# Kernel tuning notes

Hardware: AMD Instinct MI355X
Metric: run time of the kernel (lower is better)

Reference implementation:

```python
import jax, jax.numpy as jnp
import numpy as np

N_NODES = 50000
N_EDGES = 800000


def gcn_conv(x, W, b, src, dst, n):
    """PyG-style GCNConv: add self-loops, symmetric deg normalization,
    out[i] = sum_{j->i} deg[i]^-1/2 deg[j]^-1/2 (x @ W)[j] + b."""
    h = x @ W                                   # [n, d_out]
    loop = jnp.arange(n, dtype=src.dtype)
    s = jnp.concatenate([src, loop])            # sources incl self-loops
    d = jnp.concatenate([dst, loop])            # destinations incl self-loops
    deg = jax.ops.segment_sum(jnp.ones_like(d, dtype=h.dtype), d, num_segments=n)
    dinv = jax.lax.rsqrt(jnp.maximum(deg, 1.0))
    norm = dinv[s] * dinv[d]                    # [E+n]
    msg = norm[:, None] * h[s]                  # gather + scale, [E+n, d_out]
    out = jax.ops.segment_sum(msg, d, num_segments=n)  # scatter-add
    return out + b


def setup_inputs() -> dict:
    key = jax.random.key(0)
    ks = jax.random.split(key, 8)
    x = jax.random.normal(ks[0], (N_NODES, 128), dtype=jnp.float32)
    edge_index = jax.random.randint(ks[1], (2, N_EDGES), 0, N_NODES, dtype=jnp.int64)
    def glorot(k, shape):
        lim = np.sqrt(6.0 / (shape[0] + shape[1])).astype(np.float32)
        return jax.random.uniform(k, shape, dtype=jnp.float32, minval=-lim, maxval=lim)
    return {
        "x": x,
        "edge_index": edge_index,
        "W1": glorot(ks[2], (128, 128)), "b1": jnp.zeros((128,), jnp.float32),
        "W2": glorot(ks[3], (128, 64)),  "b2": jnp.zeros((64,), jnp.float32),
        "W3": glorot(ks[4], (64, 16)),   "b3": jnp.zeros((16,), jnp.float32),
    }


def reference(x, edge_index, W1, b1, W2, b2, W3, b3):
    src, dst = edge_index[0], edge_index[1]
    n = x.shape[0]
    # base_model: 2-layer GCN
    h = gcn_conv(x, W1, b1, src, dst, n)
    h = jax.nn.relu(h)
    h = gcn_conv(h, W2, b2, src, dst, n)
    # added layer + softmax over class dim
    logits = gcn_conv(h, W3, b3, src, dst, n)
    return jax.nn.softmax(logits, axis=1)
```

## Files before the change

### kernel.cpp

```cpp
#include <hip/hip_runtime.h>
#include <hip/hip_fp16.h>

#define CAP 64


__global__ __launch_bounds__(256) void k_scatter_p(const int* __restrict__ src,
                                                   const int* __restrict__ dst,
                                                   int* __restrict__ cnt,
                                                   unsigned short* __restrict__ srcS,
                                                   int E) {
    int e = blockIdx.x * 256 + threadIdx.x;
    if (e >= E) return;
    int d = dst[e];
    int pos = atomicAdd(&cnt[d], 1);
    if (pos < CAP) srcS[(size_t)d * CAP + pos] = (unsigned short)src[e];
}

__global__ __launch_bounds__(256) void k_dinv(const int* __restrict__ cnt,
                                              float* __restrict__ dinv, int n) {
    int i = blockIdx.x * 256 + threadIdx.x;
    if (i < n) dinv[i] = rsqrtf((float)cnt[i] + 1.0f);
}


template<int DIN, int DOUT, int TM, int TN, int KC>
__global__ __launch_bounds__(256) void k_gemm2h(const float* __restrict__ X,
                                                const float* __restrict__ W,
                                                const float* __restrict__ dinv,
                                                __half* __restrict__ Y, int n) {
    constexpr int CG = DOUT / TN;
    constexpr int RG = 256 / CG;
    constexpr int TILE_R = RG * TM;
    constexpr int NCHUNK = DIN / KC;
    constexpr int XS = KC + 4;
    __shared__ float wsh[KC * DOUT];
    __shared__ float xs[TILE_R * XS];

    const int rb = blockIdx.x * TILE_R;
    const int cg = threadIdx.x % CG;
    const int rg = threadIdx.x / CG;
    const int c0 = cg * TN;
    const int r0 = rg * TM;

    float acc[TM][TN] = {};

    for (int kc = 0; kc < NCHUNK; ++kc) {
        const int k0 = kc * KC;
        const float4* wg = reinterpret_cast<const float4*>(W + (size_t)k0 * DOUT);
        for (int i = threadIdx.x; i < KC * DOUT / 4; i += 256)
            reinterpret_cast<float4*>(wsh)[i] = wg[i];
        for (int i = threadIdx.x; i < TILE_R * KC / 4; i += 256) {
            int r = i / (KC / 4);
            int kk = (i % (KC / 4)) * 4;
            int row = rb + r;
            float4 v = {0.f, 0.f, 0.f, 0.f};
            if (row < n) v = *reinterpret_cast<const float4*>(X + (size_t)row * DIN + k0 + kk);
            *reinterpret_cast<float4*>(&xs[r * XS + kk]) = v;
        }
        __syncthreads();
#pragma unroll 4
        for (int k = 0; k < KC; ++k) {
            float wr[TN], xr[TM];
#pragma unroll
            for (int j = 0; j < TN; j += 4)
                *reinterpret_cast<float4*>(&wr[j]) =
                    *reinterpret_cast<const float4*>(&wsh[k * DOUT + c0 + j]);
#pragma unroll
            for (int i = 0; i < TM; ++i) xr[i] = xs[(r0 + i) * XS + k];
#pragma unroll
            for (int i = 0; i < TM; ++i)
#pragma unroll
                for (int j = 0; j < TN; ++j)
                    acc[i][j] = fmaf(xr[i], wr[j], acc[i][j]);
        }
        __syncthreads();
    }

#pragma unroll
    for (int i = 0; i < TM; ++i) {
        int row = rb + r0 + i;
        if (row < n) {
            float di = dinv[row];
            union { float4 f4; float2 f2[2]; __half h[8]; } u;
#pragma unroll
            for (int j = 0; j < TN; ++j) u.h[j] = __float2half_rn(acc[i][j] * di);
            __half* yp = Y + (size_t)row * DOUT + c0;
            if (TN == 8) *reinterpret_cast<float4*>(yp) = u.f4;
            else         *reinterpret_cast<float2*>(yp) = u.f2[0];
        }
    }
}


template<int DQ, int MODE>
__global__ __launch_bounds__(256) void k_gather_h(const __half* __restrict__ tmp,
                                                  const int* __restrict__ cnt,
                                                  const unsigned short* __restrict__ srcS,
                                                  const float* __restrict__ dinv,
                                                  const float* __restrict__ b,
                                                  float* __restrict__ out, int n) {
    int tid = blockIdx.x * 256 + threadIdx.x;
    int i = tid / DQ;
    if (i >= n) return;
    int c = tid % DQ;
    const float4* t4 = reinterpret_cast<const float4*>(tmp);
    float acc[8];
    {
        float4 v = t4[(size_t)i * DQ + c];
        const __half2* h = reinterpret_cast<const __half2*>(&v);
#pragma unroll
        for (int q = 0; q < 4; ++q) {
            float2 f = __half22float2(h[q]);
            acc[2 * q] = f.x; acc[2 * q + 1] = f.y;
        }
    }
    const int e1 = cnt[i];
    const unsigned short* sp = srcS + (size_t)i * CAP;
#pragma unroll 4
    for (int e = 0; e < e1; ++e) {
        int s = sp[e];
        float4 v = t4[(size_t)s * DQ + c];
        const __half2* h = reinterpret_cast<const __half2*>(&v);
#pragma unroll
        for (int q = 0; q < 4; ++q) {
            float2 f = __half22float2(h[q]);
            acc[2 * q] += f.x; acc[2 * q + 1] += f.y;
        }
    }
    const float di = dinv[i];
    float r[8];
    const float* bp = b + c * 8;
#pragma unroll
    for (int q = 0; q < 8; ++q) r[q] = di * acc[q] + bp[q];
    if (MODE == 1) {
#pragma unroll
        for (int q = 0; q < 8; ++q) r[q] = fmaxf(r[q], 0.f);
    }
    if (MODE == 2) {
        float m = r[0];
#pragma unroll
        for (int q = 1; q < 8; ++q) m = fmaxf(m, r[q]);
        m = fmaxf(m, __shfl_xor(m, 1, 2));
        float s = 0.f;
#pragma unroll
        for (int q = 0; q < 8; ++q) { r[q] = __expf(r[q] - m); s += r[q]; }
        s += __shfl_xor(s, 1, 2);
        float inv = 1.f / s;
#pragma unroll
        for (int q = 0; q < 8; ++q) r[q] *= inv;
    }
    float4* o4 = reinterpret_cast<float4*>(out + ((size_t)i * DQ + c) * 8);
    float4 w0 = {r[0], r[1], r[2], r[3]};
    float4 w1 = {r[4], r[5], r[6], r[7]};
    o4[0] = w0; o4[1] = w1;
}


extern "C" void kernel_launch(void* const* d_in, const int* in_sizes, int n_in,
                              void* d_out, int out_size, void* d_ws, size_t ws_size,
                              hipStream_t stream) {
    const float* x  = (const float*)d_in[0];
    const int*   ei = (const int*)d_in[1];
    const float* W1 = (const float*)d_in[2];
    const float* b1 = (const float*)d_in[3];
    const float* W2 = (const float*)d_in[4];
    const float* b2 = (const float*)d_in[5];
    const float* W3 = (const float*)d_in[6];
    const float* b3 = (const float*)d_in[7];

    const int n = in_sizes[0] / 128;
    const int E = in_sizes[1] / 2;
    const int* srcp = ei;
    const int* dstp = ei + E;

    auto align = [](size_t v) { return (v + 255) & ~(size_t)255; };
    char* ws = (char*)d_ws;
    size_t o = 0;
    float*          dinv = (float*)(ws + o);          o += align((size_t)n * 4);
    int*            cnt  = (int*)(ws + o);            o += align((size_t)n * 4);
    unsigned short* srcS = (unsigned short*)(ws + o); o += align((size_t)n * CAP * 2);
    __half*         bufA = (__half*)(ws + o);         o += align((size_t)n * 128 * 2);
    float*          bufB = (float*)(ws + o);

    auto cdiv = [](long long a, long long b) { return (int)((a + b - 1) / b); };

    hipMemsetAsync(cnt, 0, (size_t)n * 4, stream);
    k_scatter_p<<<cdiv(E, 256), 256, 0, stream>>>(srcp, dstp, cnt, srcS, E);
    k_dinv<<<cdiv(n, 256), 256, 0, stream>>>(cnt, dinv, n);

    k_gemm2h<128, 128, 4, 8, 64><<<cdiv(n, 64), 256, 0, stream>>>(x, W1, dinv, bufA, n);
    k_gather_h<16, 1><<<cdiv((long long)n * 16, 256), 256, 0, stream>>>(
        bufA, cnt, srcS, dinv, b1, bufB, n);

    k_gemm2h<128, 64, 4, 4, 64><<<cdiv(n, 64), 256, 0, stream>>>(bufB, W2, dinv, bufA, n);
    k_gather_h<8, 0><<<cdiv((long long)n * 8, 256), 256, 0, stream>>>(
        bufA, cnt, srcS, dinv, b2, bufB, n);

    k_gemm2h<64, 16, 4, 4, 64><<<cdiv(n, 256), 256, 0, stream>>>(bufB, W3, dinv, bufA, n);
    k_gather_h<2, 2><<<cdiv((long long)n * 2, 256), 256, 0, stream>>>(
        bufA, cnt, srcS, dinv, b3, (float*)d_out, n);
}
```

Baseline: 254.3 us.

## Fuse edge scatter into first GEMM launch and defer dinv scaling

The edge bucketing scatter and the first-layer GEMM now run in one launch, with block ranges split by role, so the atomic-heavy scatter overlaps with the GEMM compute. The GEMM no longer depends on dinv. A new kernel computes dinv and rescales the fp16 GEMM output in place. The GEMM K-chunk also shrinks from 64 to 32, lowering shared memory use. The trade-off is an extra read-modify-write pass over the fp16 buffer and a second fp16 rounding of the intermediate values.

```diff
diff --git a/kernel.cpp b/kernel.cpp
--- a/kernel.cpp
+++ b/kernel.cpp
@@ -4,22 +4,107 @@
 #define CAP 64
 
 
-__global__ __launch_bounds__(256) void k_scatter_p(const int* __restrict__ src,
-                                                   const int* __restrict__ dst,
-                                                   int* __restrict__ cnt,
-                                                   unsigned short* __restrict__ srcS,
-                                                   int E) {
-    int e = blockIdx.x * 256 + threadIdx.x;
-    if (e >= E) return;
-    int d = dst[e];
-    int pos = atomicAdd(&cnt[d], 1);
-    if (pos < CAP) srcS[(size_t)d * CAP + pos] = (unsigned short)src[e];
-}
-
-__global__ __launch_bounds__(256) void k_dinv(const int* __restrict__ cnt,
-                                              float* __restrict__ dinv, int n) {
-    int i = blockIdx.x * 256 + threadIdx.x;
-    if (i < n) dinv[i] = rsqrtf((float)cnt[i] + 1.0f);
+template<int DIN, int DOUT, int TM, int TN, int KC, int EPB>
+__global__ __launch_bounds__(256) void k_fused1(const float* __restrict__ X,
+                                                const float* __restrict__ W,
+                                                __half* __restrict__ Y, int n, int G_gemm,
+                                                const int* __restrict__ src,
+                                                const int* __restrict__ dst,
+                                                int* __restrict__ cnt,
+                                                unsigned short* __restrict__ srcS, int E) {
+    constexpr int CG = DOUT / TN;
+    constexpr int RG = 256 / CG;
+    constexpr int TILE_R = RG * TM;
+    constexpr int NCHUNK = DIN / KC;
+    constexpr int XS = KC + 4;
+    __shared__ float wsh[KC * DOUT];
+    __shared__ float xs[TILE_R * XS];
+
+    if (blockIdx.x >= G_gemm) {
+        int base = (blockIdx.x - G_gemm) * 256 * EPB + threadIdx.x;
+#pragma unroll
+        for (int k = 0; k < EPB; ++k) {
+            int e = base + k * 256;
+            if (e < E) {
+                int d = dst[e];
+                int pos = atomicAdd(&cnt[d], 1);
+                if (pos < CAP) srcS[(size_t)d * CAP + pos] = (unsigned short)src[e];
+            }
+        }
+        return;
+    }
+
+    const int rb = blockIdx.x * TILE_R;
+    const int cg = threadIdx.x % CG;
+    const int rg = threadIdx.x / CG;
+    const int c0 = cg * TN;
+    const int r0 = rg * TM;
+
+    float acc[TM][TN] = {};
+
+    for (int kc = 0; kc < NCHUNK; ++kc) {
+        const int k0 = kc * KC;
+        const float4* wg = reinterpret_cast<const float4*>(W + (size_t)k0 * DOUT);
+        for (int i = threadIdx.x; i < KC * DOUT / 4; i += 256)
+            reinterpret_cast<float4*>(wsh)[i] = wg[i];
+        for (int i = threadIdx.x; i < TILE_R * KC / 4; i += 256) {
+            int r = i / (KC / 4);
+            int kk = (i % (KC / 4)) * 4;
+            int row = rb + r;
+            float4 v = {0.f, 0.f, 0.f, 0.f};
+            if (row < n) v = *reinterpret_cast<const float4*>(X + (size_t)row * DIN + k0 + kk);
+            *reinterpret_cast<float4*>(&xs[r * XS + kk]) = v;
+        }
+        __syncthreads();
+#pragma unroll 4
+        for (int k = 0; k < KC; ++k) {
+            float wr[TN], xr[TM];
+#pragma unroll
+            for (int j = 0; j < TN; j += 4)
+                *reinterpret_cast<float4*>(&wr[j]) =
+                    *reinterpret_cast<const float4*>(&wsh[k * DOUT + c0 + j]);
+#pragma unroll
+            for (int i = 0; i < TM; ++i) xr[i] = xs[(r0 + i) * XS + k];
+#pragma unroll
+            for (int i = 0; i < TM; ++i)
+#pragma unroll
+                for (int j = 0; j < TN; ++j)
+                    acc[i][j] = fmaf(xr[i], wr[j], acc[i][j]);
+        }
+        __syncthreads();
+    }
+
+#pragma unroll
+    for (int i = 0; i < TM; ++i) {
+        int row = rb + r0 + i;
+        if (row < n) {
+            union { float4 f4; __half h[8]; } u;
+#pragma unroll
+            for (int j = 0; j < TN; ++j) u.h[j] = __float2half_rn(acc[i][j]);
+            *reinterpret_cast<float4*>(Y + (size_t)row * DOUT + c0) = u.f4;
+        }
+    }
+}
+
+
+__global__ __launch_bounds__(256) void k_dinv_scale(const int* __restrict__ cnt,
+                                                    float* __restrict__ dinv,
+                                                    __half* __restrict__ t, int n) {
+    int tid = blockIdx.x * 256 + threadIdx.x;
+    int i = tid / 16;
+    if (i >= n) return;
+    int c = tid % 16;
+    float di = rsqrtf((float)cnt[i] + 1.0f);
+    if (c == 0) dinv[i] = di;
+    float4 v = reinterpret_cast<float4*>(t)[(size_t)i * 16 + c];
+    __half2* h = reinterpret_cast<__half2*>(&v);
+#pragma unroll
+    for (int q = 0; q < 4; ++q) {
+        float2 f = __half22float2(h[q]);
+        f.x *= di; f.y *= di;
+        h[q] = __float22half2_rn(f);
+    }
+    reinterpret_cast<float4*>(t)[(size_t)i * 16 + c] = v;
 }
 
 
@@ -185,10 +270,14 @@
     auto cdiv = [](long long a, long long b) { return (int)((a + b - 1) / b); };
 
     hipMemsetAsync(cnt, 0, (size_t)n * 4, stream);
-    k_scatter_p<<<cdiv(E, 256), 256, 0, stream>>>(srcp, dstp, cnt, srcS, E);
-    k_dinv<<<cdiv(n, 256), 256, 0, stream>>>(cnt, dinv, n);
-
-    k_gemm2h<128, 128, 4, 8, 64><<<cdiv(n, 64), 256, 0, stream>>>(x, W1, dinv, bufA, n);
+
+    const int G_gemm = cdiv(n, 64);
+    const int G_scat = cdiv(E, 256 * 2);
+    k_fused1<128, 128, 4, 8, 32, 2><<<G_gemm + G_scat, 256, 0, stream>>>(
+        x, W1, bufA, n, G_gemm, srcp, dstp, cnt, srcS, E);
+
+    k_dinv_scale<<<cdiv((long long)n * 16, 256), 256, 0, stream>>>(cnt, dinv, bufA, n);
+
     k_gather_h<16, 1><<<cdiv((long long)n * 16, 256), 256, 0, stream>>>(
         bufA, cnt, srcS, dinv, b1, bufB, n);
 
```

After: 222.6 us. 12.4% less time.

## Fuse edge scatter into first GEMM and gather-aggregation into next-layer GEMMs

Applied to the files above, without the earlier changes.

Runs the edge bucketing as extra blocks of the first GEMM launch and drops the separate dinv kernel. Degree normalization is now computed inline with rsqrt from the counts, and the source-side dinv is applied per edge during the layer-1 gather. Layers 1 and 2 aggregate into shared memory and immediately multiply by the next weight matrix, so fp32 intermediate activations never go to global memory. This cuts the launch count from eight kernels to four and removes those round trips. The cost is one extra cnt lookup per edge in the first gather, and a first GEMM with a smaller K chunk.

```diff
diff --git a/kernel.cpp b/kernel.cpp
--- a/kernel.cpp
+++ b/kernel.cpp
@@ -4,30 +4,14 @@
 #define CAP 64
 
 
-__global__ __launch_bounds__(256) void k_scatter_p(const int* __restrict__ src,
-                                                   const int* __restrict__ dst,
-                                                   int* __restrict__ cnt,
-                                                   unsigned short* __restrict__ srcS,
-                                                   int E) {
-    int e = blockIdx.x * 256 + threadIdx.x;
-    if (e >= E) return;
-    int d = dst[e];
-    int pos = atomicAdd(&cnt[d], 1);
-    if (pos < CAP) srcS[(size_t)d * CAP + pos] = (unsigned short)src[e];
-}
-
-__global__ __launch_bounds__(256) void k_dinv(const int* __restrict__ cnt,
-                                              float* __restrict__ dinv, int n) {
-    int i = blockIdx.x * 256 + threadIdx.x;
-    if (i < n) dinv[i] = rsqrtf((float)cnt[i] + 1.0f);
-}
-
-
-template<int DIN, int DOUT, int TM, int TN, int KC>
-__global__ __launch_bounds__(256) void k_gemm2h(const float* __restrict__ X,
+template<int DIN, int DOUT, int TM, int TN, int KC, int EPB>
+__global__ __launch_bounds__(256) void k_fused1(const float* __restrict__ X,
                                                 const float* __restrict__ W,
-                                                const float* __restrict__ dinv,
-                                                __half* __restrict__ Y, int n) {
+                                                __half* __restrict__ Y, int n, int G_gemm,
+                                                const int* __restrict__ src,
+                                                const int* __restrict__ dst,
+                                                int* __restrict__ cnt,
+                                                unsigned short* __restrict__ srcS, int E) {
     constexpr int CG = DOUT / TN;
     constexpr int RG = 256 / CG;
     constexpr int TILE_R = RG * TM;
@@ -35,6 +19,20 @@
     constexpr int XS = KC + 4;
     __shared__ float wsh[KC * DOUT];
     __shared__ float xs[TILE_R * XS];
+
+    if (blockIdx.x >= G_gemm) {
+        int base = (blockIdx.x - G_gemm) * 256 * EPB + threadIdx.x;
+#pragma unroll
+        for (int k = 0; k < EPB; ++k) {
+            int e = base + k * 256;
+            if (e < E) {
+                int d = dst[e];
+                int pos = atomicAdd(&cnt[d], 1);
+                if (pos < CAP) srcS[(size_t)d * CAP + pos] = (unsigned short)src[e];
+            }
+        }
+        return;
+    }
 
     const int rb = blockIdx.x * TILE_R;
     const int cg = threadIdx.x % CG;
@@ -80,78 +78,222 @@
     for (int i = 0; i < TM; ++i) {
         int row = rb + r0 + i;
         if (row < n) {
-            float di = dinv[row];
-            union { float4 f4; float2 f2[2]; __half h[8]; } u;
-#pragma unroll
-            for (int j = 0; j < TN; ++j) u.h[j] = __float2half_rn(acc[i][j] * di);
-            __half* yp = Y + (size_t)row * DOUT + c0;
-            if (TN == 8) *reinterpret_cast<float4*>(yp) = u.f4;
-            else         *reinterpret_cast<float2*>(yp) = u.f2[0];
-        }
-    }
-}
-
-
-template<int DQ, int MODE>
-__global__ __launch_bounds__(256) void k_gather_h(const __half* __restrict__ tmp,
+            union { float4 f4; __half h[8]; } u;
+#pragma unroll
+            for (int j = 0; j < TN; ++j) u.h[j] = __float2half_rn(acc[i][j]);
+            *reinterpret_cast<float4*>(Y + (size_t)row * DOUT + c0) = u.f4;
+        }
+    }
+}
+
+
+__global__ __launch_bounds__(256) void k_g1_gemm2(const __half* __restrict__ t1,
                                                   const int* __restrict__ cnt,
                                                   const unsigned short* __restrict__ srcS,
-                                                  const float* __restrict__ dinv,
-                                                  const float* __restrict__ b,
-                                                  float* __restrict__ out, int n) {
+                                                  const float* __restrict__ b1,
+                                                  const float* __restrict__ W2,
+                                                  __half* __restrict__ t2, int n) {
+    __shared__ float h_sh[32][132];
+    __shared__ float wsh[32 * 64];
+    const int rb = blockIdx.x * 32;
+    const int tid = threadIdx.x;
+    const int c = tid & 15;
+    const int gl = tid >> 4;
+
+    for (int pass = 0; pass < 2; ++pass) {
+        const int lrow = pass * 16 + gl;
+        const int i = rb + lrow;
+        if (i < n) {
+            const int ci = cnt[i];
+            const float di = rsqrtf((float)ci + 1.0f);
+            float acc[8];
+            float4 v = reinterpret_cast<const float4*>(t1)[(size_t)i * 16 + c];
+            const __half2* hp = reinterpret_cast<const __half2*>(&v);
+#pragma unroll
+            for (int q = 0; q < 4; ++q) {
+                float2 f = __half22float2(hp[q]);
+                acc[2 * q] = di * f.x; acc[2 * q + 1] = di * f.y;
+            }
+            const int e1 = min(ci, CAP);
+            const unsigned short* sp = srcS + (size_t)i * CAP;
+#pragma unroll 4
+            for (int e = 0; e < e1; ++e) {
+                int s = sp[e];
+                float ds = rsqrtf((float)cnt[s] + 1.0f);
+                float4 w = reinterpret_cast<const float4*>(t1)[(size_t)s * 16 + c];
+                const __half2* wp = reinterpret_cast<const __half2*>(&w);
+#pragma unroll
+                for (int q = 0; q < 4; ++q) {
+                    float2 f = __half22float2(wp[q]);
+                    acc[2 * q]     = fmaf(ds, f.x, acc[2 * q]);
+                    acc[2 * q + 1] = fmaf(ds, f.y, acc[2 * q + 1]);
+                }
+            }
+#pragma unroll
+            for (int q = 0; q < 8; ++q) {
+                float r = fmaf(di, acc[q], b1[c * 8 + q]);
+                h_sh[lrow][c * 8 + q] = fmaxf(r, 0.f);
+            }
+        } else {
+#pragma unroll
+            for (int q = 0; q < 8; ++q) h_sh[lrow][c * 8 + q] = 0.f;
+        }
+    }
+    __syncthreads();
+
+    const int c0 = (tid & 15) * 4;
+    const int r0 = (tid >> 4) * 2;
+    float facc[2][4] = {};
+    for (int kc = 0; kc < 4; ++kc) {
+        const float4* wg = reinterpret_cast<const float4*>(W2 + (size_t)kc * 32 * 64);
+        reinterpret_cast<float4*>(wsh)[tid]       = wg[tid];
+        reinterpret_cast<float4*>(wsh)[tid + 256] = wg[tid + 256];
+        __syncthreads();
+#pragma unroll 8
+        for (int k = 0; k < 32; ++k) {
+            float4 wr = *reinterpret_cast<const float4*>(&wsh[k * 64 + c0]);
+            float x0 = h_sh[r0][kc * 32 + k];
+            float x1 = h_sh[r0 + 1][kc * 32 + k];
+            facc[0][0] = fmaf(x0, wr.x, facc[0][0]); facc[0][1] = fmaf(x0, wr.y, facc[0][1]);
+            facc[0][2] = fmaf(x0, wr.z, facc[0][2]); facc[0][3] = fmaf(x0, wr.w, facc[0][3]);
+            facc[1][0] = fmaf(x1, wr.x, facc[1][0]); facc[1][1] = fmaf(x1, wr.y, facc[1][1]);
+            facc[1][2] = fmaf(x1, wr.z, facc[1][2]); facc[1][3] = fmaf(x1, wr.w, facc[1][3]);
+        }
+        __syncthreads();
+    }
+#pragma unroll
+    for (int i = 0; i < 2; ++i) {
+        int row = rb + r0 + i;
+        if (row < n) {
+            float di = rsqrtf((float)cnt[row] + 1.0f);
+            union { float2 f2; __half h[4]; } u;
+#pragma unroll
+            for (int j = 0; j < 4; ++j) u.h[j] = __float2half_rn(di * facc[i][j]);
+            *reinterpret_cast<float2*>(t2 + (size_t)row * 64 + c0) = u.f2;
+        }
+    }
+}
+
+
+__global__ __launch_bounds__(256) void k_g2_gemm3(const __half* __restrict__ t2,
+                                                  const int* __restrict__ cnt,
+                                                  const unsigned short* __restrict__ srcS,
+                                                  const float* __restrict__ b2,
+                                                  const float* __restrict__ W3,
+                                                  __half* __restrict__ t3, int n) {
+    __shared__ float h_sh[32][68];
+    __shared__ float wsh[64 * 16];
+    const int rb = blockIdx.x * 32;
+    const int tid = threadIdx.x;
+    const int c = tid & 7;
+    const int g = tid >> 3;
+    const int i = rb + g;
+    if (i < n) {
+        const int ci = cnt[i];
+        const float di = rsqrtf((float)ci + 1.0f);
+        float acc[8];
+        float4 v = reinterpret_cast<const float4*>(t2)[(size_t)i * 8 + c];
+        const __half2* hp = reinterpret_cast<const __half2*>(&v);
+#pragma unroll
+        for (int q = 0; q < 4; ++q) {
+            float2 f = __half22float2(hp[q]);
+            acc[2 * q] = f.x; acc[2 * q + 1] = f.y;
+        }
+        const int e1 = min(ci, CAP);
+        const unsigned short* sp = srcS + (size_t)i * CAP;
+#pragma unroll 4
+        for (int e = 0; e < e1; ++e) {
+            int s = sp[e];
+            float4 w = reinterpret_cast<const float4*>(t2)[(size_t)s * 8 + c];
+            const __half2* wp = reinterpret_cast<const __half2*>(&w);
+#pragma unroll
+            for (int q = 0; q < 4; ++q) {
+                float2 f = __half22float2(wp[q]);
+                acc[2 * q] += f.x; acc[2 * q + 1] += f.y;
+            }
+        }
+#pragma unroll
+        for (int q = 0; q < 8; ++q)
+            h_sh[g][c * 8 + q] = fmaf(di, acc[q], b2[c * 8 + q]);
+    } else {
+#pragma unroll
+        for (int q = 0; q < 8; ++q) h_sh[g][c * 8 + q] = 0.f;
+    }
+    __syncthreads();
+    reinterpret_cast<float4*>(wsh)[tid] = reinterpret_cast<const float4*>(W3)[tid];
+    __syncthreads();
+
+    const int row = tid >> 3;
+    const int col2 = (tid & 7) * 2;
+    float a0 = 0.f, a1 = 0.f;
+#pragma unroll 8
+    for (int k = 0; k < 64; ++k) {
+        float x = h_sh[row][k];
+        a0 = fmaf(x, wsh[k * 16 + col2], a0);
+        a1 = fmaf(x, wsh[k * 16 + col2 + 1], a1);
+    }
+    int grow = rb + row;
+    if (grow < n) {
+        float di = rsqrtf((float)cnt[grow] + 1.0f);
+        union { unsigned int u32; __half h[2]; } u;
+        u.h[0] = __float2half_rn(di * a0);
+        u.h[1] = __float2half_rn(di * a1);
+        *reinterpret_cast<unsigned int*>(t3 + (size_t)grow * 16 + col2) = u.u32;
+    }
+}
+
+
+__global__ __launch_bounds__(256) void k_g3_softmax(const __half* __restrict__ t3,
+                                                    const int* __restrict__ cnt,
+                                                    const unsigned short* __restrict__ srcS,
+                                                    const float* __restrict__ b3,
+                                                    float* __restrict__ out, int n) {
     int tid = blockIdx.x * 256 + threadIdx.x;
-    int i = tid / DQ;
+    int i = tid >> 1;
     if (i >= n) return;
-    int c = tid % DQ;
-    const float4* t4 = reinterpret_cast<const float4*>(tmp);
+    int c = tid & 1;
+    const float4* t4 = reinterpret_cast<const float4*>(t3);
     float acc[8];
     {
-        float4 v = t4[(size_t)i * DQ + c];
-        const __half2* h = reinterpret_cast<const __half2*>(&v);
+        float4 v = t4[(size_t)i * 2 + c];
+        const __half2* hp = reinterpret_cast<const __half2*>(&v);
 #pragma unroll
         for (int q = 0; q < 4; ++q) {
-            float2 f = __half22float2(h[q]);
+            float2 f = __half22float2(hp[q]);
             acc[2 * q] = f.x; acc[2 * q + 1] = f.y;
         }
     }
-    const int e1 = cnt[i];
+    const int ci = cnt[i];
+    const float di = rsqrtf((float)ci + 1.0f);
+    const int e1 = min(ci, CAP);
     const unsigned short* sp = srcS + (size_t)i * CAP;
 #pragma unroll 4
     for (int e = 0; e < e1; ++e) {
         int s = sp[e];
-        float4 v = t4[(size_t)s * DQ + c];
-        const __half2* h = reinterpret_cast<const __half2*>(&v);
+        float4 v = t4[(size_t)s * 2 + c];
+        const __half2* hp = reinterpret_cast<const __half2*>(&v);
 #pragma unroll
         for (int q = 0; q < 4; ++q) {
-            float2 f = __half22float2(h[q]);
+            float2 f = __half22float2(hp[q]);
             acc[2 * q] += f.x; acc[2 * q + 1] += f.y;
         }
     }
-    const float di = dinv[i];
     float r[8];
-    const float* bp = b + c * 8;
-#pragma unroll
-    for (int q = 0; q < 8; ++q) r[q] = di * acc[q] + bp[q];
-    if (MODE == 1) {
-#pragma unroll
-        for (int q = 0; q < 8; ++q) r[q] = fmaxf(r[q], 0.f);
-    }
-    if (MODE == 2) {
-        float m = r[0];
-#pragma unroll
-        for (int q = 1; q < 8; ++q) m = fmaxf(m, r[q]);
-        m = fmaxf(m, __shfl_xor(m, 1, 2));
-        float s = 0.f;
-#pragma unroll
-        for (int q = 0; q < 8; ++q) { r[q] = __expf(r[q] - m); s += r[q]; }
-        s += __shfl_xor(s, 1, 2);
-        float inv = 1.f / s;
-#pragma unroll
-        for (int q = 0; q < 8; ++q) r[q] *= inv;
-    }
-    float4* o4 = reinterpret_cast<float4*>(out + ((size_t)i * DQ + c) * 8);
-    float4 w0 = {r[0], r[1], r[2], r[3]};
-    float4 w1 = {r[4], r[5], r[6], r[7]};
+    const float* bp = b3 + c * 8;
+#pragma unroll
+    for (int q = 0; q < 8; ++q) r[q] = fmaf(di, acc[q], bp[q]);
+    float m = r[0];
+#pragma unroll
+    for (int q = 1; q < 8; ++q) m = fmaxf(m, r[q]);
+    m = fmaxf(m, __shfl_xor(m, 1, 2));
+    float s = 0.f;
+#pragma unroll
+    for (int q = 0; q < 8; ++q) { r[q] = __expf(r[q] - m); s += r[q]; }
+    s += __shfl_xor(s, 1, 2);
+    float inv = 1.f / s;
+    float4* o4 = reinterpret_cast<float4*>(out + ((size_t)i * 2 + c) * 8);
+    float4 w0 = {r[0] * inv, r[1] * inv, r[2] * inv, r[3] * inv};
+    float4 w1 = {r[4] * inv, r[5] * inv, r[6] * inv, r[7] * inv};
     o4[0] = w0; o4[1] = w1;
 }
 
@@ -176,27 +318,25 @@
     auto align = [](size_t v) { return (v + 255) & ~(size_t)255; };
     char* ws = (char*)d_ws;
     size_t o = 0;
-    float*          dinv = (float*)(ws + o);          o += align((size_t)n * 4);
     int*            cnt  = (int*)(ws + o);            o += align((size_t)n * 4);
     unsigned short* srcS = (unsigned short*)(ws + o); o += align((size_t)n * CAP * 2);
-    __half*         bufA = (__half*)(ws + o);         o += align((size_t)n * 128 * 2);
-    float*          bufB = (float*)(ws + o);
+    __half*         t1   = (__half*)(ws + o);         o += align((size_t)n * 128 * 2);
+    __half*         t2   = (__half*)(ws + o);         o += align((size_t)n * 64 * 2);
+    __half*         t3   = (__half*)(ws + o);         o += align((size_t)n * 16 * 2);
 
     auto cdiv = [](long long a, long long b) { return (int)((a + b - 1) / b); };
 
     hipMemsetAsync(cnt, 0, (size_t)n * 4, stream);
-    k_scatter_p<<<cdiv(E, 256), 256, 0, stream>>>(srcp, dstp, cnt, srcS, E);
-    k_dinv<<<cdiv(n, 256), 256, 0, stream>>>(cnt, dinv, n);
-
-    k_gemm2h<128, 128, 4, 8, 64><<<cdiv(n, 64), 256, 0, stream>>>(x, W1, dinv, bufA, n);
-    k_gather_h<16, 1><<<cdiv((long long)n * 16, 256), 256, 0, stream>>>(
-        bufA, cnt, srcS, dinv, b1, bufB, n);
-
-    k_gemm2h<128, 64, 4, 4, 64><<<cdiv(n, 64), 256, 0, stream>>>(bufB, W2, dinv, bufA, n);
-    k_gather_h<8, 0><<<cdiv((long long)n * 8, 256), 256, 0, stream>>>(
-        bufA, cnt, srcS, dinv, b2, bufB, n);
-
-    k_gemm2h<64, 16, 4, 4, 64><<<cdiv(n, 256), 256, 0, stream>>>(bufB, W3, dinv, bufA, n);
-    k_gather_h<2, 2><<<cdiv((long long)n * 2, 256), 256, 0, stream>>>(
-        bufA, cnt, srcS, dinv, b3, (float*)d_out, n);
-}
+
+    const int G_gemm = cdiv(n, 64);
+    const int G_scat = cdiv(E, 256 * 2);
+    k_fused1<128, 128, 4, 8, 32, 2><<<G_gemm + G_scat, 256, 0, stream>>>(
+        x, W1, t1, n, G_gemm, srcp, dstp, cnt, srcS, E);
+
+    k_g1_gemm2<<<cdiv(n, 32), 256, 0, stream>>>(t1, cnt, srcS, b1, W2, t2, n);
+
+    k_g2_gemm3<<<cdiv(n, 32), 256, 0, stream>>>(t2, cnt, srcS, b2, W3, t3, n);
+
+    k_g3_softmax<<<cdiv((long long)n * 2, 256), 256, 0, stream>>>(
+        t3, cnt, srcS, b3, (float*)d_out, n);
+}
```

New measurement: 205.7 us (median of 2 runs). -19.1%, faster.
